# Performance work log

Measured on AMD Instinct MI355X. Metric: run time of the kernel, lower is better.

Reference implementation:

```python
import jax, jax.numpy as jnp
import numpy as np

EPS_GN = 1e-5
DEN_MIN = 1e-4

B, C, H, W = 16, 256, 128, 128
MEM, NH = 64, 4
HD = MEM // NH
GROUPS = min(8, C // 4)


def setup_inputs() -> dict:
    key = jax.random.key(0)
    ks = jax.random.split(key, 12)
    s = 0.02
    x = jax.random.normal(ks[0], (B, C, H, W), jnp.float32)
    gn_w = jnp.ones((C,), jnp.float32)
    gn_b = jnp.zeros((C,), jnp.float32)
    Wk = jax.random.normal(ks[1], (MEM, C), jnp.float32) * s
    Wv = jax.random.normal(ks[2], (MEM, C), jnp.float32) * s
    Wq = jax.random.normal(ks[3], (MEM, C), jnp.float32) * s
    Wo = jax.random.normal(ks[4], (C, MEM), jnp.float32) * s
    bo = jnp.zeros((C,), jnp.float32)
    M0 = jax.random.normal(ks[5], (NH, HD, HD), jnp.float32) * s  # meta-learned warm start
    Z0 = jnp.ones((NH, HD), jnp.float32) * 0.1
    g1_w = jax.random.normal(ks[6], (C // 4, C), jnp.float32) * s
    g1_b = jnp.zeros((C // 4,), jnp.float32)
    g2_w = jax.random.normal(ks[7], (1, C // 4), jnp.float32) * s
    g2_b = jnp.full((1,), -2.0, jnp.float32)  # gate_bias
    return {"x": x, "gn_w": gn_w, "gn_b": gn_b, "Wk": Wk, "Wv": Wv, "Wq": Wq,
            "Wo": Wo, "bo": bo, "M0": M0, "Z0": Z0,
            "g1_w": g1_w, "g1_b": g1_b, "g2_w": g2_w, "g2_b": g2_b}


def _group_norm(x, w, b):
    b_, c, h, wd = x.shape
    xg = x.reshape(b_, GROUPS, c // GROUPS, h, wd)
    mu = jnp.mean(xg, axis=(2, 3, 4), keepdims=True)
    var = jnp.var(xg, axis=(2, 3, 4), keepdims=True)
    xn = ((xg - mu) * jax.lax.rsqrt(var + EPS_GN)).reshape(b_, c, h, wd)
    return xn * w[None, :, None, None] + b[None, :, None, None]


def _conv1x1(x, w):
    # x: (B,C,H,W), w: (O,C) -> (B,O,H,W)
    return jnp.einsum('bchw,oc->bohw', x, w)


def reference(x, gn_w, gn_b, Wk, Wv, Wq, Wo, bo, M0, Z0, g1_w, g1_b, g2_w, g2_b):
    bsz, c, h, w = x.shape
    n = h * w
    residual = x
    x_norm = _group_norm(x, gn_w, gn_b)

    k = _conv1x1(x_norm, Wk).reshape(bsz, NH, HD, n)
    v = _conv1x1(x_norm, Wv).reshape(bsz, NH, HD, n)
    q = _conv1x1(x_norm, Wq).reshape(bsz, NH, HD, n)

    phi_k = jax.nn.elu(k) + 1.0
    phi_q = jax.nn.elu(q) + 1.0

    M = jnp.einsum('bhdn,bhen->bhde', phi_k, v) + M0[None]
    Z = phi_k.sum(axis=-1) + Z0[None]
    y_num = jnp.einsum('bhde,bhdn->bhen', M, phi_q)
    y_den = jnp.einsum('bhd,bhdn->bhn', Z, phi_q)
    y_den = jnp.maximum(y_den, DEN_MIN)[:, :, None, :]
    y = (y_num / y_den).reshape(bsz, MEM, h, w)

    y = _conv1x1(y, Wo) + bo[None, :, None, None]

    # gate: global avg pool -> Linear -> GELU (exact) -> Linear -> sigmoid
    pooled = jnp.mean(x_norm, axis=(2, 3))  # (B, C)
    g = jax.nn.gelu(pooled @ g1_w.T + g1_b, approximate=False)
    gate = jax.nn.sigmoid(g @ g2_w.T + g2_b).reshape(bsz, 1, 1, 1)

    return residual + gate * y, gate
```

## Files before the change

kernel.cpp:

```cpp
#include <hip/hip_runtime.h>
#include <math.h>

typedef __attribute__((ext_vector_type(8))) short short8b;
typedef __attribute__((ext_vector_type(4))) float f32x4;

#define B_   16
#define C_   256
#define N_   16384
#define NH_  4
#define G_   8
#define CPG_ 32

#define OFF_S    0
#define OFF_T    4096
#define OFF_SUM  OFF_S
#define OFF_SQ   OFF_T
#define OFF_M    8192
#define OFF_Z    24576
#define OFF_GATE 25600
#define OFF_WKVQ 25616

static __device__ inline unsigned short bf16u(float f) {
    unsigned int u = __float_as_uint(f);
    return (unsigned short)((u + 0x7FFFu + ((u >> 16) & 1u)) >> 16);
}
static __device__ inline float ubf(unsigned short u) {
    return __uint_as_float(((unsigned int)u) << 16);
}

__global__ __launch_bounds__(256) void k_stats(const float* __restrict__ x,
                                               float* __restrict__ ws) {
    const int bc = blockIdx.x;
    const float4* p4 = (const float4*)(x + (size_t)bc * N_);
    float s = 0.f, q = 0.f;
    #pragma unroll 4
    for (int i = threadIdx.x; i < N_ / 4; i += 256) {
        float4 v = p4[i];
        s += v.x + v.y + v.z + v.w;
        q += v.x * v.x + v.y * v.y + v.z * v.z + v.w * v.w;
    }
    #pragma unroll
    for (int o = 32; o > 0; o >>= 1) {
        s += __shfl_down(s, o);
        q += __shfl_down(q, o);
    }
    __shared__ float ls[4], lq[4];
    const int wid = threadIdx.x >> 6, lane = threadIdx.x & 63;
    if (lane == 0) { ls[wid] = s; lq[wid] = q; }
    __syncthreads();
    if (threadIdx.x == 0) {
        ws[OFF_SUM + bc] = ls[0] + ls[1] + ls[2] + ls[3];
        ws[OFF_SQ  + bc] = lq[0] + lq[1] + lq[2] + lq[3];
    }
}

__global__ __launch_bounds__(256) void k_cvtw(const float* __restrict__ Wk,
        const float* __restrict__ Wv, const float* __restrict__ Wq,
        float* __restrict__ ws) {
    unsigned short* wkvq = (unsigned short*)(ws + OFF_WKVQ);
    const int r = blockIdx.x, t = threadIdx.x;
    const float* src = r < 64 ? Wk + r * C_
                     : r < 128 ? Wv + (r - 64) * C_
                     : Wq + (r - 128) * C_;
    wkvq[r * 256 + t] = bf16u(src[t]);
}

__global__ __launch_bounds__(256) void k_prep(
        const float* __restrict__ gnw, const float* __restrict__ gnb,
        const float* __restrict__ M0,  const float* __restrict__ Z0,
        const float* __restrict__ g1w, const float* __restrict__ g1b,
        const float* __restrict__ g2w, const float* __restrict__ g2b,
        float* __restrict__ ws, float* __restrict__ out_gate) {
    const int b = blockIdx.x, t = threadIdx.x;
    __shared__ float mu[G_], rs[G_];
    __shared__ float pooled[C_];
    __shared__ float hidden[64];

    if (t < G_) {
        float S = 0.f, Q = 0.f;
        for (int c = t * CPG_; c < (t + 1) * CPG_; ++c) {
            S += ws[OFF_SUM + b * C_ + c];
            Q += ws[OFF_SQ  + b * C_ + c];
        }
        const float cnt = (float)(CPG_ * N_);
        const float m = S / cnt;
        const float var = Q / cnt - m * m;
        mu[t] = m;
        rs[t] = rsqrtf(var + 1e-5f);
    }
    __syncthreads();
    {
        const int c = t;
        const int g = c / CPG_;
        const float sumc = ws[OFF_SUM + b * C_ + c];
        const float sc = rs[g] * gnw[c];
        const float tc = gnb[c] - mu[g] * sc;
        ws[OFF_S + b * C_ + c] = sc;
        ws[OFF_T + b * C_ + c] = tc;
        pooled[c] = fmaf(sumc * (1.f / (float)N_), sc, tc);
    }
    __syncthreads();
    if (t < 64) {
        float a = g1b[t];
        for (int c = 0; c < C_; ++c) a = fmaf(pooled[c], g1w[t * C_ + c], a);
        hidden[t] = 0.5f * a * (1.f + erff(a * 0.70710678118654752f));
    }
    __syncthreads();
    if (t == 0) {
        float z = g2b[0];
        for (int j = 0; j < 64; ++j) z = fmaf(hidden[j], g2w[j], z);
        const float gate = 1.f / (1.f + expf(-z));
        ws[OFF_GATE + b] = gate;
        out_gate[b] = gate;
    }
    for (int i = t; i < NH_ * 256; i += 256) ws[OFF_M + b * 1024 + i] = M0[i];
    for (int i = t; i < 64;        i += 256) ws[OFF_Z + b * 64 + i]   = Z0[i];
}

__global__ __launch_bounds__(256) void k_projmz(const float* __restrict__ x,
                                                float* __restrict__ ws) {
    __shared__ __align__(16) char lds[35072];
    char* w_s = lds;
    char* x_s = lds + 10240;
    unsigned short (*kvt)[136] = (unsigned short (*)[136])lds;
    float* z_red = (float*)(lds + 34816);

    const int b = blockIdx.y, px0 = blockIdx.x * 128;
    const int t = threadIdx.x, w = t >> 6, l = t & 63;
    const int stag = blockIdx.x & 7;
    const float* __restrict__ sv = ws + OFF_S + b * C_;
    const float* __restrict__ tv = ws + OFF_T + b * C_;
    const unsigned int* __restrict__ wkvq32 = (const unsigned int*)(ws + OFF_WKVQ);
    const float* __restrict__ xb = x + (size_t)b * C_ * N_ + px0;

    if (t < 64) z_red[t] = 0.f;

    f32x4 acc[2][8];
    #pragma unroll
    for (int i = 0; i < 2; ++i)
        #pragma unroll
        for (int j = 0; j < 8; ++j) acc[i][j] = (f32x4){0.f, 0.f, 0.f, 0.f};

    for (int kk = 0; kk < 8; ++kk) {
        const int ks = (stag + kk) & 7;
        __syncthreads();
        #pragma unroll
        for (int i = 0; i < 8; ++i) {
            const int e2 = t + 256 * i;
            const int row = e2 >> 4, kp = e2 & 15;
            *(unsigned int*)(w_s + row * 80 + kp * 4) =
                wkvq32[row * 128 + ks * 16 + kp];
        }
        {
            const int px = t & 127, half = t >> 7;
            #pragma unroll
            for (int i = 0; i < 8; ++i) {
                const int lc = half * 16 + i * 2;
                const int c = ks * 32 + lc;
                const float a0 = fmaf(xb[(size_t)c * N_ + px],       sv[c],     tv[c]);
                const float a1 = fmaf(xb[(size_t)(c + 1) * N_ + px], sv[c + 1], tv[c + 1]);
                *(unsigned int*)(x_s + px * 80 + lc * 2) =
                    ((unsigned int)bf16u(a1) << 16) | bf16u(a0);
            }
        }
        __syncthreads();
        short8b bfr[8];
        #pragma unroll
        for (int ct = 0; ct < 8; ++ct)
            bfr[ct] = *(const short8b*)(x_s + (ct * 16 + (l & 15)) * 80 + (l >> 4) * 16);
        #pragma unroll
        for (int rt = 0; rt < 2; ++rt) {
            const int row = w * 32 + rt * 16 + (l & 15);
            const short8b af = *(const short8b*)(w_s + row * 80 + (l >> 4) * 16);
            #pragma unroll
            for (int ct = 0; ct < 8; ++ct)
                acc[rt][ct] = __builtin_amdgcn_mfma_f32_16x16x32_bf16(
                                  af, bfr[ct], acc[rt][ct], 0, 0, 0);
        }
    }
    __syncthreads();

    #pragma unroll
    for (int rt = 0; rt < 2; ++rt) {
        const int base = w * 32 + rt * 16;
        const bool do_elu = base < 64;
        #pragma unroll
        for (int ct = 0; ct < 8; ++ct) {
            const int px = ct * 16 + (l & 15);
            #pragma unroll
            for (int r = 0; r < 4; ++r) {
                const int row = base + (l >> 4) * 4 + r;
                float v = acc[rt][ct][r];
                if (do_elu) v = v > 0.f ? v + 1.f : __expf(v);
                kvt[row][px] = bf16u(v);
            }
        }
    }
    __syncthreads();

    f32x4 accm = (f32x4){0.f, 0.f, 0.f, 0.f};
    #pragma unroll
    for (int kc = 0; kc < 4; ++kc) {
        const short8b af = *(const short8b*)((const char*)&kvt[w * 16 + (l & 15)][0]
                                             + kc * 64 + (l >> 4) * 16);
        const short8b bf = *(const short8b*)((const char*)&kvt[64 + w * 16 + (l & 15)][0]
                                             + kc * 64 + (l >> 4) * 16);
        accm = __builtin_amdgcn_mfma_f32_16x16x32_bf16(af, bf, accm, 0, 0, 0);
    }
    {
        const int zrow = t >> 2, zq = t & 3;
        float z = 0.f;
        #pragma unroll
        for (int j = 0; j < 16; ++j) {
            const unsigned int u = *(const unsigned int*)&kvt[zrow][zq * 32 + j * 2];
            z += ubf((unsigned short)u) + ubf((unsigned short)(u >> 16));
        }
        atomicAdd(&z_red[zrow], z);
    }
    #pragma unroll
    for (int r = 0; r < 4; ++r) {
        const int d = (l >> 4) * 4 + r, e = l & 15;
        atomicAdd(&ws[OFF_M + b * 1024 + w * 256 + d * 16 + e], accm[r]);
    }
    __syncthreads();
    if (t < 64) atomicAdd(&ws[OFF_Z + b * 64 + t], z_red[t]);
}

__global__ __launch_bounds__(512, 4) void k_out5(const float* __restrict__ x,
        const float* __restrict__ Wo, const float* __restrict__ bo,
        const float* __restrict__ ws, float* __restrict__ out) {
    __shared__ __align__(16) char lds[74752];
    char*  pq_s = lds;
    char*  breg = lds + 32768;
    float* bo_s = (float*)(lds + 73728);

    const int b = blockIdx.y, px0 = blockIdx.x * 256;
    const int t = threadIdx.x, w = t >> 6, l = t & 63;
    const int h = w >> 1;
    const int pxw = (w & 1) * 128;
    const int stag = blockIdx.x & 7;
    const float* __restrict__ sv = ws + OFF_S + b * C_;
    const float* __restrict__ tv = ws + OFF_T + b * C_;
    const unsigned short* __restrict__ wkvq16 = (const unsigned short*)(ws + OFF_WKVQ);
    const float* __restrict__ xb = x + (size_t)b * C_ * N_ + px0;

    if (t < 256) bo_s[t] = bo[t];
    float* m_s = (float*)pq_s;
    for (int i = t; i < 1024; i += 512) m_s[i] = ws[OFF_M + b * 1024 + i];
    float zr[4];
    #pragma unroll
    for (int r = 0; r < 4; ++r)
        zr[r] = ws[OFF_Z + b * 64 + h * 16 + (l >> 4) * 4 + r];

    short8b afq[8];
    {
        const unsigned short* wq = wkvq16
            + (size_t)(128 + h * 16 + (l & 15)) * 256 + (l >> 4) * 8;
        #pragma unroll
        for (int kk = 0; kk < 8; ++kk)
            afq[kk] = *(const short8b*)(wq + ((stag + kk) & 7) * 32);
    }

    const int px_ = t & 255, half = t >> 8;
    char* xs0 = breg;
    char* xs1 = breg + 20480;

    f32x4 accq[8];
    #pragma unroll
    for (int j = 0; j < 8; ++j) accq[j] = (f32x4){0.f, 0.f, 0.f, 0.f};

    {
        float xf[16];
        #pragma unroll
        for (int i = 0; i < 16; ++i)
            xf[i] = xb[(size_t)(stag * 32 + half * 16 + i) * N_ + px_];
        #pragma unroll
        for (int i = 0; i < 8; ++i) {
            const int c = stag * 32 + half * 16 + 2 * i;
            const float a0 = fmaf(xf[2 * i],     sv[c],     tv[c]);
            const float a1 = fmaf(xf[2 * i + 1], sv[c + 1], tv[c + 1]);
            *(unsigned int*)(xs0 + px_ * 80 + (half * 16 + 2 * i) * 2) =
                ((unsigned int)bf16u(a1) << 16) | bf16u(a0);
        }
    }
    __syncthreads();
    #pragma unroll
    for (int kk = 0; kk < 8; ++kk) {
        char* xcur = (kk & 1) ? xs1 : xs0;
        char* xnxt = (kk & 1) ? xs0 : xs1;
        const int ksn = (stag + kk + 1) & 7;
        float xg[16];
        if (kk < 7) {
            #pragma unroll
            for (int i = 0; i < 16; ++i)
                xg[i] = xb[(size_t)(ksn * 32 + half * 16 + i) * N_ + px_];
        }
        #pragma unroll
        for (int ct = 0; ct < 8; ++ct) {
            const short8b bfr = *(const short8b*)(xcur + (pxw + ct * 16 + (l & 15)) * 80
                                                  + (l >> 4) * 16);
            accq[ct] = __builtin_amdgcn_mfma_f32_16x16x32_bf16(
                           afq[kk], bfr, accq[ct], 0, 0, 0);
        }
        if (kk < 7) {
            #pragma unroll
            for (int i = 0; i < 8; ++i) {
                const int c = ksn * 32 + half * 16 + 2 * i;
                const float a0 = fmaf(xg[2 * i],     sv[c],     tv[c]);
                const float a1 = fmaf(xg[2 * i + 1], sv[c + 1], tv[c + 1]);
                *(unsigned int*)(xnxt + px_ * 80 + (half * 16 + 2 * i) * 2) =
                    ((unsigned int)bf16u(a1) << 16) | bf16u(a0);
            }
        }
        __syncthreads();
    }

    char* w2_s = breg;
    {
        const int c = t & 255, hp = t >> 8;
        #pragma unroll
        for (int hh = 0; hh < 2; ++hh) {
            const int hw = hp * 2 + hh;
            float wrow[16];
            #pragma unroll
            for (int j = 0; j < 4; ++j)
                *(float4*)&wrow[j * 4] = *(const float4*)&Wo[c * 64 + hw * 16 + j * 4];
            float av[16];
            #pragma unroll
            for (int d = 0; d < 16; ++d) {
                float a = 0.f;
                #pragma unroll
                for (int e = 0; e < 16; ++e)
                    a = fmaf(wrow[e], m_s[hw * 256 + d * 16 + e], a);
                av[d] = a;
            }
            #pragma unroll
            for (int j = 0; j < 8; ++j) {
                const unsigned int pk = (unsigned int)bf16u(av[2 * j])
                                      | ((unsigned int)bf16u(av[2 * j + 1]) << 16);
                *(unsigned int*)(w2_s + c * 128 + ((hw * 32 + j * 4) ^ ((c & 7) << 4))) = pk;
            }
        }
    }
    __syncthreads();

    #pragma unroll
    for (int ct = 0; ct < 8; ++ct) {
        float p[4];
        #pragma unroll
        for (int r = 0; r < 4; ++r) {
            const float v = accq[ct][r];
            p[r] = v > 0.f ? v + 1.f : __expf(v);
        }
        float dp = 0.f;
        #pragma unroll
        for (int r = 0; r < 4; ++r) dp = fmaf(zr[r], p[r], dp);
        dp += __shfl_xor(dp, 16);
        dp += __shfl_xor(dp, 32);
        const float rd = 1.f / fmaxf(dp, 1e-4f);
        const int px = pxw + ct * 16 + (l & 15);
        const unsigned int lo = (unsigned int)bf16u(p[0] * rd)
                              | ((unsigned int)bf16u(p[1] * rd) << 16);
        const unsigned int hi = (unsigned int)bf16u(p[2] * rd)
                              | ((unsigned int)bf16u(p[3] * rd) << 16);
        const int off = (h * 32 + (l >> 4) * 8) ^ ((px & 7) << 4);
        *(unsigned long long*)(pq_s + px * 128 + off) =
            (unsigned long long)lo | ((unsigned long long)hi << 32);
    }
    __syncthreads();

    const float gate = ws[OFF_GATE + b];
    const float* __restrict__ xr = x + (size_t)b * C_ * N_ + px0;
    float* __restrict__ ob = out + (size_t)b * C_ * N_ + px0;
    #pragma unroll
    for (int rti = 0; rti < 4; ++rti) {
        const int rt = (rti + blockIdx.x) & 3;
        f32x4 acc[8];
        #pragma unroll
        for (int j = 0; j < 8; ++j) acc[j] = (f32x4){0.f, 0.f, 0.f, 0.f};
        const int row = h * 64 + rt * 16 + (l & 15);
        #pragma unroll
        for (int ksi = 0; ksi < 2; ++ksi) {
            const short8b af = *(const short8b*)(w2_s + row * 128
                                 + ((ksi * 64 + (l >> 4) * 16) ^ ((row & 7) << 4)));
            #pragma unroll
            for (int ct = 0; ct < 8; ++ct) {
                const int px = pxw + ct * 16 + (l & 15);
                const short8b bfr = *(const short8b*)(pq_s + px * 128
                                 + ((ksi * 64 + (l >> 4) * 16) ^ ((px & 7) << 4)));
                acc[ct] = __builtin_amdgcn_mfma_f32_16x16x32_bf16(
                              af, bfr, acc[ct], 0, 0, 0);
            }
        }
        #pragma unroll
        for (int ct = 0; ct < 8; ++ct) {
            const int px = pxw + ct * 16 + (l & 15);
            #pragma unroll
            for (int r = 0; r < 4; ++r) {
                const int orow = h * 64 + rt * 16 + (l >> 4) * 4 + r;
                const size_t off = (size_t)orow * N_ + px;
                ob[off] = fmaf(gate, acc[ct][r] + bo_s[orow], xr[off]);
            }
        }
    }
}

extern "C" void kernel_launch(void* const* d_in, const int* in_sizes, int n_in,
                              void* d_out, int out_size, void* d_ws, size_t ws_size,
                              hipStream_t stream) {
    const float* x   = (const float*)d_in[0];
    const float* gnw = (const float*)d_in[1];
    const float* gnb = (const float*)d_in[2];
    const float* Wk  = (const float*)d_in[3];
    const float* Wv  = (const float*)d_in[4];
    const float* Wq  = (const float*)d_in[5];
    const float* Wo  = (const float*)d_in[6];
    const float* bo  = (const float*)d_in[7];
    const float* M0  = (const float*)d_in[8];
    const float* Z0  = (const float*)d_in[9];
    const float* g1w = (const float*)d_in[10];
    const float* g1b = (const float*)d_in[11];
    const float* g2w = (const float*)d_in[12];
    const float* g2b = (const float*)d_in[13];
    float* out = (float*)d_out;
    float* ws  = (float*)d_ws;

    hipLaunchKernelGGL(k_stats,  dim3(B_ * C_), dim3(256), 0, stream, x, ws);
    hipLaunchKernelGGL(k_cvtw,   dim3(192),     dim3(256), 0, stream, Wk, Wv, Wq, ws);
    hipLaunchKernelGGL(k_prep,   dim3(B_),      dim3(256), 0, stream,
                       gnw, gnb, M0, Z0, g1w, g1b, g2w, g2b, ws,
                       out + (size_t)B_ * C_ * N_);
    hipLaunchKernelGGL(k_projmz, dim3(N_ / 128, B_), dim3(256), 0, stream, x, ws);
    hipLaunchKernelGGL(k_out5,   dim3(N_ / 256, B_), dim3(512), 0, stream,
                       x, Wo, bo, ws, out);
}
```

Measured before the change: 289.3 us.

## Process batch in chunks of four so x stays resident in last-level cache

```diff
diff --git a/kernel.cpp b/kernel.cpp
--- a/kernel.cpp
+++ b/kernel.cpp
@@ -10,6 +10,7 @@
 #define NH_  4
 #define G_   8
 #define CPG_ 32
+#define BCH_ 4
 
 #define OFF_S    0
 #define OFF_T    4096
@@ -29,8 +30,8 @@
 }
 
 __global__ __launch_bounds__(256) void k_stats(const float* __restrict__ x,
-                                               float* __restrict__ ws) {
-    const int bc = blockIdx.x;
+                                               float* __restrict__ ws, int b0) {
+    const int bc = b0 * C_ + blockIdx.x;
     const float4* p4 = (const float4*)(x + (size_t)bc * N_);
     float s = 0.f, q = 0.f;
     #pragma unroll 4
@@ -70,8 +71,8 @@
         const float* __restrict__ M0,  const float* __restrict__ Z0,
         const float* __restrict__ g1w, const float* __restrict__ g1b,
         const float* __restrict__ g2w, const float* __restrict__ g2b,
-        float* __restrict__ ws, float* __restrict__ out_gate) {
-    const int b = blockIdx.x, t = threadIdx.x;
+        float* __restrict__ ws, float* __restrict__ out_gate, int b0) {
+    const int b = b0 + blockIdx.x, t = threadIdx.x;
     __shared__ float mu[G_], rs[G_];
     __shared__ float pooled[C_];
     __shared__ float hidden[64];
@@ -118,14 +119,14 @@
 }
 
 __global__ __launch_bounds__(256) void k_projmz(const float* __restrict__ x,
-                                                float* __restrict__ ws) {
+                                                float* __restrict__ ws, int b0) {
     __shared__ __align__(16) char lds[35072];
     char* w_s = lds;
     char* x_s = lds + 10240;
     unsigned short (*kvt)[136] = (unsigned short (*)[136])lds;
     float* z_red = (float*)(lds + 34816);
 
-    const int b = blockIdx.y, px0 = blockIdx.x * 128;
+    const int b = b0 + blockIdx.y, px0 = blockIdx.x * 128;
     const int t = threadIdx.x, w = t >> 6, l = t & 63;
     const int stag = blockIdx.x & 7;
     const float* __restrict__ sv = ws + OFF_S + b * C_;
@@ -228,13 +229,13 @@
 
 __global__ __launch_bounds__(512, 4) void k_out5(const float* __restrict__ x,
         const float* __restrict__ Wo, const float* __restrict__ bo,
-        const float* __restrict__ ws, float* __restrict__ out) {
+        const float* __restrict__ ws, float* __restrict__ out, int b0) {
     __shared__ __align__(16) char lds[74752];
     char*  pq_s = lds;
     char*  breg = lds + 32768;
     float* bo_s = (float*)(lds + 73728);
 
-    const int b = blockIdx.y, px0 = blockIdx.x * 256;
+    const int b = b0 + blockIdx.y, px0 = blockIdx.x * 256;
     const int t = threadIdx.x, w = t >> 6, l = t & 63;
     const int h = w >> 1;
     const int pxw = (w & 1) * 128;
@@ -425,12 +426,17 @@
     float* out = (float*)d_out;
     float* ws  = (float*)d_ws;
 
-    hipLaunchKernelGGL(k_stats,  dim3(B_ * C_), dim3(256), 0, stream, x, ws);
-    hipLaunchKernelGGL(k_cvtw,   dim3(192),     dim3(256), 0, stream, Wk, Wv, Wq, ws);
-    hipLaunchKernelGGL(k_prep,   dim3(B_),      dim3(256), 0, stream,
-                       gnw, gnb, M0, Z0, g1w, g1b, g2w, g2b, ws,
-                       out + (size_t)B_ * C_ * N_);
-    hipLaunchKernelGGL(k_projmz, dim3(N_ / 128, B_), dim3(256), 0, stream, x, ws);
-    hipLaunchKernelGGL(k_out5,   dim3(N_ / 256, B_), dim3(512), 0, stream,
-                       x, Wo, bo, ws, out);
-}
+    hipLaunchKernelGGL(k_cvtw, dim3(192), dim3(256), 0, stream, Wk, Wv, Wq, ws);
+
+    for (int b0 = 0; b0 < B_; b0 += BCH_) {
+        hipLaunchKernelGGL(k_stats,  dim3(BCH_ * C_), dim3(256), 0, stream,
+                           x, ws, b0);
+        hipLaunchKernelGGL(k_prep,   dim3(BCH_),      dim3(256), 0, stream,
+                           gnw, gnb, M0, Z0, g1w, g1b, g2w, g2b, ws,
+                           out + (size_t)B_ * C_ * N_, b0);
+        hipLaunchKernelGGL(k_projmz, dim3(N_ / 128, BCH_), dim3(256), 0, stream,
+                           x, ws, b0);
+        hipLaunchKernelGGL(k_out5,   dim3(N_ / 256, BCH_), dim3(512), 0, stream,
+                           x, Wo, bo, ws, out, b0);
+    }
+}
```

Measured after the change: 372.8 us. +28.8%, slower.
